# Optimization experiments

Hardware: AMD Instinct MI355X
Metric: run time of the kernel (lower is better)

## Reference

```python
import jax, jax.numpy as jnp
import numpy as np

N_NODES = 50000
N_EDGES = 800000
DIM_IN, DIM_H, DIM_OUT = 96, 128, 16


def setup_inputs() -> dict:
    key = jax.random.key(0)
    ks = jax.random.split(key, 8)
    x = jax.random.normal(ks[0], (N_NODES, DIM_IN), dtype=jnp.float32)
    edge_index = jax.random.randint(ks[1], (2, N_EDGES), 0, N_NODES, dtype=jnp.int64)
    W1_l = jax.random.normal(ks[2], (DIM_IN, DIM_H), dtype=jnp.float32) * 0.1
    b1_l = jax.random.normal(ks[3], (DIM_H,), dtype=jnp.float32) * 0.1
    W1_r = jax.random.normal(ks[4], (DIM_IN, DIM_H), dtype=jnp.float32) * 0.1
    W2_l = jax.random.normal(ks[5], (DIM_H, DIM_OUT), dtype=jnp.float32) * 0.1
    b2_l = jax.random.normal(ks[6], (DIM_OUT,), dtype=jnp.float32) * 0.1
    W2_r = jax.random.normal(ks[7], (DIM_H, DIM_OUT), dtype=jnp.float32) * 0.1
    return {"x": x, "edge_index": edge_index, "W1_l": W1_l, "b1_l": b1_l,
            "W1_r": W1_r, "W2_l": W2_l, "b2_l": b2_l, "W2_r": W2_r}


def _mean_aggregate(x, src, dst, n_nodes):
    # gather neighbor features along edges, mean-reduce at destination nodes
    msgs = x[src]                                      # [E, d]
    agg = jax.ops.segment_sum(msgs, dst, num_segments=n_nodes)  # [N, d]
    deg = jax.ops.segment_sum(jnp.ones_like(src, dtype=x.dtype), dst,
                              num_segments=n_nodes)    # [N]
    return agg / jnp.maximum(deg, 1.0)[:, None]


def _sage_conv(x, src, dst, W_l, b_l, W_r):
    # PyG SAGEConv (mean aggr): lin_l(mean_j x_j) + lin_r(x); bias on lin_l only
    agg = _mean_aggregate(x, src, dst, x.shape[0])
    return agg @ W_l + b_l + x @ W_r


def reference(x, edge_index, W1_l, b1_l, W1_r, W2_l, b2_l, W2_r):
    src, dst = edge_index[0], edge_index[1]
    h = jax.nn.relu(_sage_conv(x, src, dst, W1_l, b1_l, W1_r))
    h = _sage_conv(h, src, dst, W2_l, b2_l, W2_r)
    return jax.nn.softmax(h, axis=1)
```

## Files before the change

### kernel.cpp

```cpp
#include <hip/hip_runtime.h>

#define NN 50000
#define NE 800000
#define DIN 96
#define DH 128
#define DOUT 16
#define NBKT ((NN + 127) / 128)
#define CAP 2560
#define EPB 8192

typedef __attribute__((ext_vector_type(8))) short bf16x8;
typedef __attribute__((ext_vector_type(4))) float f32x4;
typedef unsigned short ushort_t;

__device__ inline short f2bf(float f) {
    unsigned u = __float_as_uint(f);
    u += 0x7fff + ((u >> 16) & 1);
    return (short)(u >> 16);
}
__device__ inline float bflo(unsigned u) { return __uint_as_float(u << 16); }
__device__ inline float bfhi(unsigned u) { return __uint_as_float(u & 0xffff0000u); }

#define XB_BLOCKS ((NN * DIN / 4 + 255) / 256)
#define WC_BLOCKS ((DH * 192 + 32 * DH + 255) / 256)
__global__ __launch_bounds__(256) void k_prep(const float* __restrict__ x,
                                              const float* __restrict__ W1l,
                                              const float* __restrict__ W1r,
                                              const float* __restrict__ W2l,
                                              const float* __restrict__ W2r,
                                              short* __restrict__ xb,
                                              short* __restrict__ Bt,
                                              short* __restrict__ Bt2,
                                              int* __restrict__ gbcur) {
    if (blockIdx.x < XB_BLOCKS) {
        int i = blockIdx.x * 256 + threadIdx.x;
        if (i < NN * DIN / 4) {
            float4 v = ((const float4*)x)[i];
            short4 o;
            o.x = f2bf(v.x); o.y = f2bf(v.y); o.z = f2bf(v.z); o.w = f2bf(v.w);
            ((short4*)xb)[i] = o;
        }
    } else if (blockIdx.x < XB_BLOCKS + WC_BLOCKS) {
        int idx = (blockIdx.x - XB_BLOCKS) * 256 + threadIdx.x;
        if (idx < DH * 192) {
            int n = idx / 192, kk = idx % 192;
            float v = (kk < DIN) ? W1l[kk * DH + n] : W1r[(kk - DIN) * DH + n];
            Bt[idx] = f2bf(v);
        } else if (idx < DH * 192 + 32 * DH) {
            int j = idx - DH * 192;
            int c = j >> 7, k = j & 127;
            float v = (c < DOUT) ? W2l[k * DOUT + c] : W2r[k * DOUT + (c - DOUT)];
            Bt2[j] = f2bf(v);
        }
    } else {
        for (int i = threadIdx.x; i < NBKT; i += 256) gbcur[i] = 0;
    }
}

__global__ __launch_bounds__(512) void k_bucket(const int* __restrict__ ei,
                                                int* __restrict__ gbcur,
                                                unsigned* __restrict__ bpack) {
    __shared__ unsigned stage[EPB];
    __shared__ int bcnt[NBKT];
    __shared__ int bfil[NBKT];
    __shared__ int brun[NBKT];
    __shared__ int bres[NBKT];
    __shared__ int sbuf[512];
    const int tid = threadIdx.x;
    const int e0 = blockIdx.x * EPB;
    const int ecnt = min(EPB, NE - e0);

    for (int i = tid; i < NBKT; i += 512) { bcnt[i] = 0; bfil[i] = 0; }
    __syncthreads();
    unsigned dcache[EPB / 512];
#pragma unroll
    for (int k = 0; k < EPB / 512; ++k) {
        int i = tid + k * 512;
        if (i < ecnt) {
            unsigned d = (unsigned)ei[NE + e0 + i];
            dcache[k] = d;
            atomicAdd(&bcnt[d >> 7], 1);
        }
    }
    __syncthreads();
    int v = (tid < NBKT) ? bcnt[tid] : 0;
    sbuf[tid] = v;
    __syncthreads();
    for (int o = 1; o < 512; o <<= 1) {
        int tv = (tid >= o) ? sbuf[tid - o] : 0;
        __syncthreads();
        sbuf[tid] += tv;
        __syncthreads();
    }
    if (tid < NBKT) brun[tid] = sbuf[tid] - v;
    __syncthreads();
#pragma unroll
    for (int k = 0; k < EPB / 512; ++k) {
        int i = tid + k * 512;
        if (i < ecnt) {
            unsigned s = (unsigned)ei[e0 + i];
            unsigned d = dcache[k];
            int b = d >> 7;
            int p = atomicAdd(&bfil[b], 1);
            stage[brun[b] + p] = (d << 16) | s;
        }
    }
    __syncthreads();
    for (int b = tid; b < NBKT; b += 512) {
        int n = bcnt[b];
        bres[b] = n ? atomicAdd(&gbcur[b], n) : 0;
    }
    __syncthreads();
    for (int i = tid; i < ecnt; i += 512) {
        unsigned p = stage[i];
        int b = p >> 23;
        int idx = bres[b] + (i - brun[b]);
        if (idx < CAP)
            bpack[(size_t)b * CAP + idx] = p;
    }
}

__global__ __launch_bounds__(256) void k_bfill(const unsigned* __restrict__ bpack,
                                               const int* __restrict__ gbcur,
                                               int* __restrict__ offs,
                                               int* __restrict__ offe,
                                               ushort_t* __restrict__ csr) {
    __shared__ unsigned stage[CAP];
    __shared__ int ncnt[128];
    __shared__ int nrun[128];
    __shared__ int lcur[128];
    __shared__ int buf[256];
    const int b = blockIdx.x;
    const int tid = threadIdx.x;
    const int pb = b * CAP;
    const int cnt = min(gbcur[b], CAP);
    if (tid < 128) { ncnt[tid] = 0; lcur[tid] = 0; }
    __syncthreads();
    for (int i = tid; i < cnt; i += 256) {
        unsigned p = bpack[pb + i];
        stage[i] = p;
        atomicAdd(&ncnt[(p >> 16) & 127], 1);
    }
    __syncthreads();
    int v = (tid < 128) ? ncnt[tid] : 0;
    buf[tid] = v;
    __syncthreads();
    for (int o = 1; o < 128; o <<= 1) {
        int tv = (tid >= o) ? buf[tid - o] : 0;
        __syncthreads();
        buf[tid] += tv;
        __syncthreads();
    }
    if (tid < 128) {
        nrun[tid] = buf[tid] - v;
        const int n = b * 128 + tid;
        if (n < NN) {
            offs[n] = pb + nrun[tid];
            offe[n] = pb + nrun[tid] + v;
        }
    }
    __syncthreads();
    for (int i = tid; i < cnt; i += 256) {
        unsigned p = stage[i];
        int nd = (p >> 16) & 127;
        int pos = atomicAdd(&lcur[nd], 1);
        csr[pb + nrun[nd] + pos] = (ushort_t)(p & 0xffffu);
    }
}

__global__ __launch_bounds__(256) void k_agg1(const short* __restrict__ xb,
                                              const ushort_t* __restrict__ csr,
                                              const int* __restrict__ offs,
                                              const int* __restrict__ offe,
                                              short* __restrict__ m1b) {
    const int w = threadIdx.x >> 6;
    const int l = threadIdx.x & 63;
    const int n = blockIdx.x * 4 + w;
    if (n >= NN) return;
    const int eg = l / 12;
    const int c  = l % 12;
    const int b = offs[n], e = offe[n];
    const float4* xq = (const float4*)xb;
    float acc[8];
#pragma unroll
    for (int k = 0; k < 8; ++k) acc[k] = 0.f;
    int i = (eg < 4) ? b + eg : e;
    for (; i + 12 < e; i += 16) {
        int s0 = csr[i], s1 = csr[i + 4], s2 = csr[i + 8], s3 = csr[i + 12];
        float4 v0 = xq[(size_t)s0 * 12 + c];
        float4 v1 = xq[(size_t)s1 * 12 + c];
        float4 v2 = xq[(size_t)s2 * 12 + c];
        float4 v3 = xq[(size_t)s3 * 12 + c];
        const unsigned* u0 = (const unsigned*)&v0;
        const unsigned* u1 = (const unsigned*)&v1;
        const unsigned* u2 = (const unsigned*)&v2;
        const unsigned* u3 = (const unsigned*)&v3;
#pragma unroll
        for (int j = 0; j < 4; ++j) {
            acc[2 * j]     += (bflo(u0[j]) + bflo(u1[j])) + (bflo(u2[j]) + bflo(u3[j]));
            acc[2 * j + 1] += (bfhi(u0[j]) + bfhi(u1[j])) + (bfhi(u2[j]) + bfhi(u3[j]));
        }
    }
    for (; i < e; i += 4) {
        float4 v0 = xq[(size_t)csr[i] * 12 + c];
        const unsigned* u0 = (const unsigned*)&v0;
#pragma unroll
        for (int j = 0; j < 4; ++j) {
            acc[2 * j]     += bflo(u0[j]);
            acc[2 * j + 1] += bfhi(u0[j]);
        }
    }
#pragma unroll
    for (int k = 0; k < 8; ++k) acc[k] += __shfl(acc[k], l + 24);
#pragma unroll
    for (int k = 0; k < 8; ++k) acc[k] += __shfl(acc[k], l + 12);
    if (l < 12) {
        const float inv = (e > b) ? 1.0f / (float)(e - b) : 0.0f;
        uint4 o;
        unsigned* op = (unsigned*)&o;
#pragma unroll
        for (int j = 0; j < 4; ++j)
            op[j] = (unsigned)(unsigned short)f2bf(acc[2 * j] * inv)
                  | ((unsigned)(unsigned short)f2bf(acc[2 * j + 1] * inv) << 16);
        ((uint4*)m1b)[(size_t)n * 12 + l] = o;
    }
}

#define SHP 136
__global__ __launch_bounds__(256) void k_linproj(const short* __restrict__ m1b,
                                                 const short* __restrict__ xb,
                                                 const short* __restrict__ Bt,
                                                 const float* __restrict__ b1,
                                                 const short* __restrict__ Bt2,
                                                 const float* __restrict__ b2,
                                                 short* __restrict__ zlb,
                                                 float* __restrict__ s) {
    __shared__ __align__(16) short sh[64][SHP];
    const int w = threadIdx.x >> 6;
    const int l = threadIdx.x & 63;
    const int lr = l & 15;
    const int lk = l >> 4;
    int row = blockIdx.x * 64 + w * 16 + lr;
    if (row >= NN) row = NN - 1;

    f32x4 acc[8];
#pragma unroll
    for (int nt = 0; nt < 8; ++nt) {
        float bv = b1[nt * 16 + lr];
        acc[nt] = (f32x4){bv, bv, bv, bv};
    }

    bf16x8 afr[6];
    {
        const bf16x8* am = (const bf16x8*)(m1b + (size_t)row * DIN);
        const bf16x8* ax = (const bf16x8*)(xb  + (size_t)row * DIN);
        afr[0] = am[lk];     afr[1] = am[4 + lk]; afr[2] = am[8 + lk];
        afr[3] = ax[lk];     afr[4] = ax[4 + lk]; afr[5] = ax[8 + lk];
    }

    const bf16x8* bt8 = (const bf16x8*)Bt;
#pragma unroll
    for (int st = 0; st < 6; ++st) {
#pragma unroll
        for (int nt = 0; nt < 8; ++nt) {
            bf16x8 bfr = bt8[(size_t)(nt * 16 + lr) * 24 + st * 4 + lk];
            acc[nt] = __builtin_amdgcn_mfma_f32_16x16x32_bf16(afr[st], bfr, acc[nt], 0, 0, 0);
        }
    }

    const int lrow0 = w * 16 + lk * 4;
#pragma unroll
    for (int r = 0; r < 4; ++r) {
#pragma unroll
        for (int nt = 0; nt < 8; ++nt)
            sh[lrow0 + r][nt * 16 + lr] = f2bf(fmaxf(acc[nt][r], 0.f));
    }
    __syncthreads();

    bf16x8 pafr[4];
#pragma unroll
    for (int st = 0; st < 4; ++st)
        pafr[st] = *(const bf16x8*)&sh[w * 16 + lr][st * 32 + lk * 8];

    f32x4 accz = (f32x4){0.f, 0.f, 0.f, 0.f};
    float bv = b2[lr];
    f32x4 accs = (f32x4){bv, bv, bv, bv};
    const bf16x8* b8 = (const bf16x8*)Bt2;
#pragma unroll
    for (int st = 0; st < 4; ++st) {
        bf16x8 bz = b8[(size_t)lr * 16 + st * 4 + lk];
        bf16x8 bs = b8[(size_t)(16 + lr) * 16 + st * 4 + lk];
        accz = __builtin_amdgcn_mfma_f32_16x16x32_bf16(pafr[st], bz, accz, 0, 0, 0);
        accs = __builtin_amdgcn_mfma_f32_16x16x32_bf16(pafr[st], bs, accs, 0, 0, 0);
    }

    const int orow0 = blockIdx.x * 64 + w * 16 + lk * 4;
#pragma unroll
    for (int r = 0; r < 4; ++r) {
        const int orow = orow0 + r;
        if (orow < NN) {
            zlb[(size_t)orow * DOUT + lr] = f2bf(accz[r]);
            s[(size_t)orow * DOUT + lr] = accs[r];
        }
    }
}

__global__ __launch_bounds__(256) void k_agg2(const short* __restrict__ zlb,
                                              const float* __restrict__ s,
                                              const ushort_t* __restrict__ csr,
                                              const int* __restrict__ offs,
                                              const int* __restrict__ offe,
                                              float* __restrict__ out) {
    const int w = threadIdx.x >> 6;
    const int lane = threadIdx.x & 63;
    const int n = blockIdx.x * 4 + w;
    if (n >= NN) return;
    const int b = offs[n], e = offe[n];
    const int ng = lane >> 2;
    const int sl = lane & 3;
    const uint2* z2 = (const uint2*)zlb;
    float4 acc = {0.f, 0.f, 0.f, 0.f};
    for (int i = b + ng; i < e; i += 16) {
        uint2 u = z2[(size_t)csr[i] * 4 + sl];
        acc.x += bflo(u.x);
        acc.y += bfhi(u.x);
        acc.z += bflo(u.y);
        acc.w += bfhi(u.y);
    }
#pragma unroll
    for (int o = 4; o <= 32; o <<= 1) {
        acc.x += __shfl_xor(acc.x, o);
        acc.y += __shfl_xor(acc.y, o);
        acc.z += __shfl_xor(acc.z, o);
        acc.w += __shfl_xor(acc.w, o);
    }
    const float inv = (e > b) ? 1.0f / (float)(e - b) : 0.0f;
    const float4 sv = ((const float4*)s)[(size_t)n * 4 + sl];
    float4 v;
    v.x = acc.x * inv + sv.x;
    v.y = acc.y * inv + sv.y;
    v.z = acc.z * inv + sv.z;
    v.w = acc.w * inv + sv.w;
    float mx = fmaxf(fmaxf(v.x, v.y), fmaxf(v.z, v.w));
    mx = fmaxf(mx, __shfl_xor(mx, 1));
    mx = fmaxf(mx, __shfl_xor(mx, 2));
    v.x = expf(v.x - mx); v.y = expf(v.y - mx);
    v.z = expf(v.z - mx); v.w = expf(v.w - mx);
    float sm = v.x + v.y + v.z + v.w;
    sm += __shfl_xor(sm, 1);
    sm += __shfl_xor(sm, 2);
    const float r = 1.0f / sm;
    v.x *= r; v.y *= r; v.z *= r; v.w *= r;
    if (ng == 0) ((float4*)out)[(size_t)n * 4 + sl] = v;
}

template <typename T>
static inline T* align_up(void* p, size_t a = 64) {
    return (T*)(((uintptr_t)p + (a - 1)) & ~(uintptr_t)(a - 1));
}

extern "C" void kernel_launch(void* const* d_in, const int* in_sizes, int n_in,
                              void* d_out, int out_size, void* d_ws, size_t ws_size,
                              hipStream_t stream) {
    const float* x   = (const float*)d_in[0];
    const int*   ei  = (const int*)d_in[1];
    const float* W1l = (const float*)d_in[2];
    const float* b1  = (const float*)d_in[3];
    const float* W1r = (const float*)d_in[4];
    const float* W2l = (const float*)d_in[5];
    const float* b2  = (const float*)d_in[6];
    const float* W2r = (const float*)d_in[7];
    float* out = (float*)d_out;

    unsigned* bpack = (unsigned*)d_ws;
    float* s      = (float*)(bpack + (size_t)NBKT * CAP);
    int* offs     = (int*)(s + (size_t)NN * DOUT);
    int* offe     = offs + NN;
    int* gbcur    = offe + NN;
    ushort_t* csr = (ushort_t*)align_up<short>(gbcur + NBKT);
    short* xb     = (short*)csr + (size_t)NBKT * CAP;
    short* m1b    = xb + (size_t)NN * DIN;
    short* zlb    = m1b + (size_t)NN * DIN;
    short* Bt     = zlb + (size_t)NN * DOUT;
    short* Bt2    = Bt + (size_t)DH * 192;

    k_prep<<<XB_BLOCKS + WC_BLOCKS + 1, 256, 0, stream>>>(
        x, W1l, W1r, W2l, W2r, xb, Bt, Bt2, gbcur);
    k_bucket<<<(NE + EPB - 1) / EPB, 512, 0, stream>>>(ei, gbcur, bpack);
    k_bfill<<<NBKT, 256, 0, stream>>>(bpack, gbcur, offs, offe, csr);

    k_agg1<<<(NN + 3) / 4, 256, 0, stream>>>(xb, csr, offs, offe, m1b);
    k_linproj<<<(NN + 63) / 64, 256, 0, stream>>>(m1b, xb, Bt, b1, Bt2, b2, zlb, s);
    k_agg2<<<(NN + 3) / 4, 256, 0, stream>>>(zlb, s, csr, offs, offe, out);
}
```

Measured before the change: 109.1 us.

## Fuse bucketing into prep and merge CSR build, layer-1 aggregation and projection

Edge bucketing moves into the prep kernel, which now writes fixed-size per-slice slots with per-slice counts, so the global atomic cursor and its zeroing go away. A new per-bucket mega kernel gathers the slices, builds the local CSR in shared memory, computes the layer-1 mean aggregation into shared memory, and runs both MFMA projections. This drops the m1b round trip through global memory and two kernel launches. The cost is a large shared-memory footprint, lower occupancy, only 391 blocks of 512 threads for the gather-heavy phase, and silent truncation of any slice with more than 52 edges in one bucket.

```diff
diff --git a/kernel.cpp b/kernel.cpp
--- a/kernel.cpp
+++ b/kernel.cpp
@@ -6,8 +6,10 @@
 #define DH 128
 #define DOUT 16
 #define NBKT ((NN + 127) / 128)
-#define CAP 2560
+#define CAPB 2560
 #define EPB 8192
+#define NSLC ((NE + EPB - 1) / EPB)
+#define SLICE 52
 
 typedef __attribute__((ext_vector_type(8))) short bf16x8;
 typedef __attribute__((ext_vector_type(4))) float f32x4;
@@ -21,27 +23,38 @@
 __device__ inline float bflo(unsigned u) { return __uint_as_float(u << 16); }
 __device__ inline float bfhi(unsigned u) { return __uint_as_float(u & 0xffff0000u); }
 
-#define XB_BLOCKS ((NN * DIN / 4 + 255) / 256)
-#define WC_BLOCKS ((DH * 192 + 32 * DH + 255) / 256)
-__global__ __launch_bounds__(256) void k_prep(const float* __restrict__ x,
+#define XB_BLOCKS ((NN * DIN / 4 + 511) / 512)
+#define WC_BLOCKS ((DH * 192 + 32 * DH + 511) / 512)
+__global__ __launch_bounds__(512) void k_prep(const float* __restrict__ x,
                                               const float* __restrict__ W1l,
                                               const float* __restrict__ W1r,
                                               const float* __restrict__ W2l,
                                               const float* __restrict__ W2r,
+                                              const int* __restrict__ ei,
                                               short* __restrict__ xb,
                                               short* __restrict__ Bt,
                                               short* __restrict__ Bt2,
-                                              int* __restrict__ gbcur) {
+                                              unsigned* __restrict__ bpack,
+                                              int* __restrict__ scnt) {
+    __shared__ unsigned stage[EPB];
+    __shared__ int bcnt[NBKT];
+    __shared__ int bfil[NBKT];
+    __shared__ int brun[NBKT];
+    __shared__ int sbuf[512];
+    const int tid = threadIdx.x;
+
     if (blockIdx.x < XB_BLOCKS) {
-        int i = blockIdx.x * 256 + threadIdx.x;
+        int i = blockIdx.x * 512 + tid;
         if (i < NN * DIN / 4) {
             float4 v = ((const float4*)x)[i];
             short4 o;
             o.x = f2bf(v.x); o.y = f2bf(v.y); o.z = f2bf(v.z); o.w = f2bf(v.w);
             ((short4*)xb)[i] = o;
         }
-    } else if (blockIdx.x < XB_BLOCKS + WC_BLOCKS) {
-        int idx = (blockIdx.x - XB_BLOCKS) * 256 + threadIdx.x;
+        return;
+    }
+    if (blockIdx.x < XB_BLOCKS + WC_BLOCKS) {
+        int idx = (blockIdx.x - XB_BLOCKS) * 512 + tid;
         if (idx < DH * 192) {
             int n = idx / 192, kk = idx % 192;
             float v = (kk < DIN) ? W1l[kk * DH + n] : W1r[(kk - DIN) * DH + n];
@@ -52,24 +65,11 @@
             float v = (c < DOUT) ? W2l[k * DOUT + c] : W2r[k * DOUT + (c - DOUT)];
             Bt2[j] = f2bf(v);
         }
-    } else {
-        for (int i = threadIdx.x; i < NBKT; i += 256) gbcur[i] = 0;
-    }
-}
-
-__global__ __launch_bounds__(512) void k_bucket(const int* __restrict__ ei,
-                                                int* __restrict__ gbcur,
-                                                unsigned* __restrict__ bpack) {
-    __shared__ unsigned stage[EPB];
-    __shared__ int bcnt[NBKT];
-    __shared__ int bfil[NBKT];
-    __shared__ int brun[NBKT];
-    __shared__ int bres[NBKT];
-    __shared__ int sbuf[512];
-    const int tid = threadIdx.x;
-    const int e0 = blockIdx.x * EPB;
+        return;
+    }
+    const int j = blockIdx.x - XB_BLOCKS - WC_BLOCKS;
+    const int e0 = j * EPB;
     const int ecnt = min(EPB, NE - e0);
-
     for (int i = tid; i < NBKT; i += 512) { bcnt[i] = 0; bfil[i] = 0; }
     __syncthreads();
     unsigned dcache[EPB / 512];
@@ -106,181 +106,205 @@
         }
     }
     __syncthreads();
-    for (int b = tid; b < NBKT; b += 512) {
-        int n = bcnt[b];
-        bres[b] = n ? atomicAdd(&gbcur[b], n) : 0;
-    }
-    __syncthreads();
     for (int i = tid; i < ecnt; i += 512) {
         unsigned p = stage[i];
         int b = p >> 23;
-        int idx = bres[b] + (i - brun[b]);
-        if (idx < CAP)
-            bpack[(size_t)b * CAP + idx] = p;
-    }
-}
-
-__global__ __launch_bounds__(256) void k_bfill(const unsigned* __restrict__ bpack,
-                                               const int* __restrict__ gbcur,
-                                               int* __restrict__ offs,
-                                               int* __restrict__ offe,
-                                               ushort_t* __restrict__ csr) {
-    __shared__ unsigned stage[CAP];
+        int idx = i - brun[b];
+        if (idx < SLICE)
+            bpack[((size_t)b * NSLC + j) * SLICE + idx] = p;
+    }
+    for (int b = tid; b < NBKT; b += 512)
+        scnt[b * NSLC + j] = min(bcnt[b], SLICE);
+}
+
+__global__ __launch_bounds__(512) void k_mega(const short* __restrict__ xb,
+                                              const unsigned* __restrict__ bpack,
+                                              const int* __restrict__ scnt,
+                                              const short* __restrict__ Bt,
+                                              const float* __restrict__ b1,
+                                              const short* __restrict__ Bt2,
+                                              const float* __restrict__ b2,
+                                              int* __restrict__ offs,
+                                              int* __restrict__ offe,
+                                              ushort_t* __restrict__ csr,
+                                              short* __restrict__ zlb,
+                                              float* __restrict__ sout) {
+    __shared__ __align__(16) char uscr[128 * 136 * 2];
+    unsigned* pairs = (unsigned*)uscr;
+    short (*ht)[136] = (short(*)[136])uscr;
+    __shared__ __align__(16) short m1t[128][104];
+    __shared__ ushort_t csr_l[CAPB];
+    __shared__ int scl[NSLC];
+    __shared__ int sbs[NSLC];
+    __shared__ int sbuf[512];
     __shared__ int ncnt[128];
     __shared__ int nrun[128];
     __shared__ int lcur[128];
-    __shared__ int buf[256];
+    __shared__ float inv_l[128];
+    __shared__ int cnt_s;
+
     const int b = blockIdx.x;
     const int tid = threadIdx.x;
-    const int pb = b * CAP;
-    const int cnt = min(gbcur[b], CAP);
+    const int w = tid >> 6;
+    const int l = tid & 63;
+
+    if (tid < NSLC) scl[tid] = scnt[b * NSLC + tid];
+    __syncthreads();
+    int v = (tid < NSLC) ? scl[tid] : 0;
+    sbuf[tid] = v;
+    __syncthreads();
+    for (int o = 1; o < 512; o <<= 1) {
+        int tv = (tid >= o) ? sbuf[tid - o] : 0;
+        __syncthreads();
+        sbuf[tid] += tv;
+        __syncthreads();
+    }
+    if (tid < NSLC) sbs[tid] = sbuf[tid] - v;
+    if (tid == NSLC - 1) cnt_s = sbuf[tid];
     if (tid < 128) { ncnt[tid] = 0; lcur[tid] = 0; }
     __syncthreads();
-    for (int i = tid; i < cnt; i += 256) {
-        unsigned p = bpack[pb + i];
-        stage[i] = p;
-        atomicAdd(&ncnt[(p >> 16) & 127], 1);
-    }
-    __syncthreads();
-    int v = (tid < 128) ? ncnt[tid] : 0;
-    buf[tid] = v;
-    __syncthreads();
-    for (int o = 1; o < 128; o <<= 1) {
-        int tv = (tid >= o) ? buf[tid - o] : 0;
-        __syncthreads();
-        buf[tid] += tv;
+    const int cnt = min(cnt_s, CAPB);
+
+    for (int idx = tid; idx < NSLC * SLICE; idx += 512) {
+        int j = idx / SLICE, k = idx - j * SLICE;
+        if (k < scl[j]) {
+            int pos = sbs[j] + k;
+            if (pos < CAPB)
+                pairs[pos] = bpack[((size_t)b * NSLC + j) * SLICE + k];
+        }
+    }
+    __syncthreads();
+
+    for (int i = tid; i < cnt; i += 512)
+        atomicAdd(&ncnt[(pairs[i] >> 16) & 127], 1);
+    __syncthreads();
+    v = (tid < 128) ? ncnt[tid] : 0;
+    sbuf[tid] = v;
+    __syncthreads();
+    for (int o = 1; o < 512; o <<= 1) {
+        int tv = (tid >= o) ? sbuf[tid - o] : 0;
+        __syncthreads();
+        sbuf[tid] += tv;
         __syncthreads();
     }
     if (tid < 128) {
-        nrun[tid] = buf[tid] - v;
+        nrun[tid] = sbuf[tid] - v;
+        inv_l[tid] = v ? 1.0f / (float)v : 0.0f;
         const int n = b * 128 + tid;
         if (n < NN) {
-            offs[n] = pb + nrun[tid];
-            offe[n] = pb + nrun[tid] + v;
-        }
-    }
-    __syncthreads();
-    for (int i = tid; i < cnt; i += 256) {
-        unsigned p = stage[i];
+            offs[n] = b * CAPB + nrun[tid];
+            offe[n] = b * CAPB + nrun[tid] + v;
+        }
+    }
+    __syncthreads();
+
+    for (int i = tid; i < cnt; i += 512) {
+        unsigned p = pairs[i];
         int nd = (p >> 16) & 127;
         int pos = atomicAdd(&lcur[nd], 1);
-        csr[pb + nrun[nd] + pos] = (ushort_t)(p & 0xffffu);
-    }
-}
-
-__global__ __launch_bounds__(256) void k_agg1(const short* __restrict__ xb,
-                                              const ushort_t* __restrict__ csr,
-                                              const int* __restrict__ offs,
-                                              const int* __restrict__ offe,
-                                              short* __restrict__ m1b) {
-    const int w = threadIdx.x >> 6;
-    const int l = threadIdx.x & 63;
-    const int n = blockIdx.x * 4 + w;
-    if (n >= NN) return;
-    const int eg = l / 12;
-    const int c  = l % 12;
-    const int b = offs[n], e = offe[n];
-    const float4* xq = (const float4*)xb;
-    float acc[8];
-#pragma unroll
-    for (int k = 0; k < 8; ++k) acc[k] = 0.f;
-    int i = (eg < 4) ? b + eg : e;
-    for (; i + 12 < e; i += 16) {
-        int s0 = csr[i], s1 = csr[i + 4], s2 = csr[i + 8], s3 = csr[i + 12];
-        float4 v0 = xq[(size_t)s0 * 12 + c];
-        float4 v1 = xq[(size_t)s1 * 12 + c];
-        float4 v2 = xq[(size_t)s2 * 12 + c];
-        float4 v3 = xq[(size_t)s3 * 12 + c];
-        const unsigned* u0 = (const unsigned*)&v0;
-        const unsigned* u1 = (const unsigned*)&v1;
-        const unsigned* u2 = (const unsigned*)&v2;
-        const unsigned* u3 = (const unsigned*)&v3;
-#pragma unroll
-        for (int j = 0; j < 4; ++j) {
-            acc[2 * j]     += (bflo(u0[j]) + bflo(u1[j])) + (bflo(u2[j]) + bflo(u3[j]));
-            acc[2 * j + 1] += (bfhi(u0[j]) + bfhi(u1[j])) + (bfhi(u2[j]) + bfhi(u3[j]));
-        }
-    }
-    for (; i < e; i += 4) {
-        float4 v0 = xq[(size_t)csr[i] * 12 + c];
-        const unsigned* u0 = (const unsigned*)&v0;
-#pragma unroll
-        for (int j = 0; j < 4; ++j) {
-            acc[2 * j]     += bflo(u0[j]);
-            acc[2 * j + 1] += bfhi(u0[j]);
-        }
-    }
-#pragma unroll
-    for (int k = 0; k < 8; ++k) acc[k] += __shfl(acc[k], l + 24);
-#pragma unroll
-    for (int k = 0; k < 8; ++k) acc[k] += __shfl(acc[k], l + 12);
-    if (l < 12) {
-        const float inv = (e > b) ? 1.0f / (float)(e - b) : 0.0f;
-        uint4 o;
-        unsigned* op = (unsigned*)&o;
-#pragma unroll
-        for (int j = 0; j < 4; ++j)
-            op[j] = (unsigned)(unsigned short)f2bf(acc[2 * j] * inv)
-                  | ((unsigned)(unsigned short)f2bf(acc[2 * j + 1] * inv) << 16);
-        ((uint4*)m1b)[(size_t)n * 12 + l] = o;
-    }
-}
-
-#define SHP 136
-__global__ __launch_bounds__(256) void k_linproj(const short* __restrict__ m1b,
-                                                 const short* __restrict__ xb,
-                                                 const short* __restrict__ Bt,
-                                                 const float* __restrict__ b1,
-                                                 const short* __restrict__ Bt2,
-                                                 const float* __restrict__ b2,
-                                                 short* __restrict__ zlb,
-                                                 float* __restrict__ s) {
-    __shared__ __align__(16) short sh[64][SHP];
-    const int w = threadIdx.x >> 6;
-    const int l = threadIdx.x & 63;
+        csr_l[nrun[nd] + pos] = (ushort_t)(p & 0xffffu);
+    }
+    __syncthreads();
+
+    for (int i = tid; i < CAPB / 2; i += 512)
+        ((int*)csr)[(size_t)b * (CAPB / 2) + i] = ((const int*)csr_l)[i];
+
+    {
+        const int eg = l / 12;
+        const int c  = l % 12;
+        const float4* xq = (const float4*)xb;
+        for (int nd = w; nd < 128; nd += 8) {
+            const int bl = nrun[nd];
+            const int deg = ncnt[nd];
+            float acc[8];
+#pragma unroll
+            for (int k = 0; k < 8; ++k) acc[k] = 0.f;
+            int i = (eg < 4) ? eg : deg;
+            for (; i + 12 < deg; i += 16) {
+                int s0 = csr_l[bl + i], s1 = csr_l[bl + i + 4];
+                int s2 = csr_l[bl + i + 8], s3 = csr_l[bl + i + 12];
+                float4 v0 = xq[(size_t)s0 * 12 + c];
+                float4 v1 = xq[(size_t)s1 * 12 + c];
+                float4 v2 = xq[(size_t)s2 * 12 + c];
+                float4 v3 = xq[(size_t)s3 * 12 + c];
+                const unsigned* u0 = (const unsigned*)&v0;
+                const unsigned* u1 = (const unsigned*)&v1;
+                const unsigned* u2 = (const unsigned*)&v2;
+                const unsigned* u3 = (const unsigned*)&v3;
+#pragma unroll
+                for (int jj = 0; jj < 4; ++jj) {
+                    acc[2 * jj]     += (bflo(u0[jj]) + bflo(u1[jj])) + (bflo(u2[jj]) + bflo(u3[jj]));
+                    acc[2 * jj + 1] += (bfhi(u0[jj]) + bfhi(u1[jj])) + (bfhi(u2[jj]) + bfhi(u3[jj]));
+                }
+            }
+            for (; i < deg; i += 4) {
+                float4 v0 = xq[(size_t)csr_l[bl + i] * 12 + c];
+                const unsigned* u0 = (const unsigned*)&v0;
+#pragma unroll
+                for (int jj = 0; jj < 4; ++jj) {
+                    acc[2 * jj]     += bflo(u0[jj]);
+                    acc[2 * jj + 1] += bfhi(u0[jj]);
+                }
+            }
+#pragma unroll
+            for (int k = 0; k < 8; ++k) acc[k] += __shfl(acc[k], l + 24);
+#pragma unroll
+            for (int k = 0; k < 8; ++k) acc[k] += __shfl(acc[k], l + 12);
+            if (l < 12) {
+                const float inv = inv_l[nd];
+                uint4 o;
+                unsigned* op = (unsigned*)&o;
+#pragma unroll
+                for (int jj = 0; jj < 4; ++jj)
+                    op[jj] = (unsigned)(unsigned short)f2bf(acc[2 * jj] * inv)
+                           | ((unsigned)(unsigned short)f2bf(acc[2 * jj + 1] * inv) << 16);
+                *(uint4*)&m1t[nd][c * 8] = o;
+            }
+        }
+    }
+    __syncthreads();
+
     const int lr = l & 15;
     const int lk = l >> 4;
-    int row = blockIdx.x * 64 + w * 16 + lr;
-    if (row >= NN) row = NN - 1;
-
-    f32x4 acc[8];
+    int row_g = b * 128 + w * 16 + lr;
+    if (row_g >= NN) row_g = NN - 1;
+
+    f32x4 acc1[8];
 #pragma unroll
     for (int nt = 0; nt < 8; ++nt) {
         float bv = b1[nt * 16 + lr];
-        acc[nt] = (f32x4){bv, bv, bv, bv};
-    }
-
+        acc1[nt] = (f32x4){bv, bv, bv, bv};
+    }
     bf16x8 afr[6];
     {
-        const bf16x8* am = (const bf16x8*)(m1b + (size_t)row * DIN);
-        const bf16x8* ax = (const bf16x8*)(xb  + (size_t)row * DIN);
+        const bf16x8* am = (const bf16x8*)&m1t[w * 16 + lr][0];
+        const bf16x8* ax = (const bf16x8*)(xb + (size_t)row_g * DIN);
         afr[0] = am[lk];     afr[1] = am[4 + lk]; afr[2] = am[8 + lk];
         afr[3] = ax[lk];     afr[4] = ax[4 + lk]; afr[5] = ax[8 + lk];
     }
-
     const bf16x8* bt8 = (const bf16x8*)Bt;
 #pragma unroll
     for (int st = 0; st < 6; ++st) {
 #pragma unroll
         for (int nt = 0; nt < 8; ++nt) {
             bf16x8 bfr = bt8[(size_t)(nt * 16 + lr) * 24 + st * 4 + lk];
-            acc[nt] = __builtin_amdgcn_mfma_f32_16x16x32_bf16(afr[st], bfr, acc[nt], 0, 0, 0);
-        }
-    }
-
+            acc1[nt] = __builtin_amdgcn_mfma_f32_16x16x32_bf16(afr[st], bfr, acc1[nt], 0, 0, 0);
+        }
+    }
+    __syncthreads();
     const int lrow0 = w * 16 + lk * 4;
 #pragma unroll
     for (int r = 0; r < 4; ++r) {
 #pragma unroll
         for (int nt = 0; nt < 8; ++nt)
-            sh[lrow0 + r][nt * 16 + lr] = f2bf(fmaxf(acc[nt][r], 0.f));
+            ht[lrow0 + r][nt * 16 + lr] = f2bf(fmaxf(acc1[nt][r], 0.f));
     }
     __syncthreads();
 
     bf16x8 pafr[4];
 #pragma unroll
     for (int st = 0; st < 4; ++st)
-        pafr[st] = *(const bf16x8*)&sh[w * 16 + lr][st * 32 + lk * 8];
+        pafr[st] = *(const bf16x8*)&ht[w * 16 + lr][st * 32 + lk * 8];
 
     f32x4 accz = (f32x4){0.f, 0.f, 0.f, 0.f};
     float bv = b2[lr];
@@ -293,14 +317,13 @@
         accz = __builtin_amdgcn_mfma_f32_16x16x32_bf16(pafr[st], bz, accz, 0, 0, 0);
         accs = __builtin_amdgcn_mfma_f32_16x16x32_bf16(pafr[st], bs, accs, 0, 0, 0);
     }
-
-    const int orow0 = blockIdx.x * 64 + w * 16 + lk * 4;
+    const int orow0 = b * 128 + w * 16 + lk * 4;
 #pragma unroll
     for (int r = 0; r < 4; ++r) {
         const int orow = orow0 + r;
         if (orow < NN) {
             zlb[(size_t)orow * DOUT + lr] = f2bf(accz[r]);
-            s[(size_t)orow * DOUT + lr] = accs[r];
+            sout[(size_t)orow * DOUT + lr] = accs[r];
         }
     }
 }
@@ -373,23 +396,19 @@
     float* out = (float*)d_out;
 
     unsigned* bpack = (unsigned*)d_ws;
-    float* s      = (float*)(bpack + (size_t)NBKT * CAP);
+    int* scnt     = (int*)(bpack + (size_t)NBKT * NSLC * SLICE);
+    float* s      = (float*)(scnt + (size_t)NBKT * NSLC);
     int* offs     = (int*)(s + (size_t)NN * DOUT);
     int* offe     = offs + NN;
-    int* gbcur    = offe + NN;
-    ushort_t* csr = (ushort_t*)align_up<short>(gbcur + NBKT);
-    short* xb     = (short*)csr + (size_t)NBKT * CAP;
-    short* m1b    = xb + (size_t)NN * DIN;
-    short* zlb    = m1b + (size_t)NN * DIN;
+    ushort_t* csr = (ushort_t*)align_up<short>(offe + NN);
+    short* xb     = (short*)csr + (size_t)NBKT * CAPB;
+    short* zlb    = xb + (size_t)NN * DIN;
     short* Bt     = zlb + (size_t)NN * DOUT;
     short* Bt2    = Bt + (size_t)DH * 192;
 
-    k_prep<<<XB_BLOCKS + WC_BLOCKS + 1, 256, 0, stream>>>(
-        x, W1l, W1r, W2l, W2r, xb, Bt, Bt2, gbcur);
-    k_bucket<<<(NE + EPB - 1) / EPB, 512, 0, stream>>>(ei, gbcur, bpack);
-    k_bfill<<<NBKT, 256, 0, stream>>>(bpack, gbcur, offs, offe, csr);
-
-    k_agg1<<<(NN + 3) / 4, 256, 0, stream>>>(xb, csr, offs, offe, m1b);
-    k_linproj<<<(NN + 63) / 64, 256, 0, stream>>>(m1b, xb, Bt, b1, Bt2, b2, zlb, s);
+    k_prep<<<XB_BLOCKS + WC_BLOCKS + NSLC, 512, 0, stream>>>(
+        x, W1l, W1r, W2l, W2r, ei, xb, Bt, Bt2, bpack, scnt);
+    k_mega<<<NBKT, 512, 0, stream>>>(xb, bpack, scnt, Bt, b1, Bt2, b2,
+                                     offs, offe, csr, zlb, s);
     k_agg2<<<(NN + 3) / 4, 256, 0, stream>>>(zlb, s, csr, offs, offe, out);
 }
```

Result: no change. 109.2 us (+0.1%).
